# Performance work log

Hardware: AMD Instinct MI355X
Metric: run time of the kernel (lower is better)

## Reference

```python
import jax, jax.numpy as jnp
import numpy as np

NUM_CLIPS = 64
# (kernel, stride) per layer for each scale, per num_scale_layers=[16,8,8]
SCALE_SPECS = [[(1, 1)] + [(2, 1)] * 15,
               [(3, 2)] + [(2, 1)] * 7,
               [(3, 2)] + [(2, 1)] * 7]
KEEP = {0: (7, 15), 1: (3, 7), 2: (3, 5, 7)}


def _build_props():
    # replicates SparsePropMaxPool.__init__ construction of self.props
    tmp = [[1] * 16, [2] + [1] * 7, [2] + [1] * 7]
    acum, stride, props = 0, 1, []
    for scale_idx, strides in enumerate(tmp):
        for i, st in enumerate(strides):
            stride *= st
            if i in KEEP[scale_idx]:
                s = np.arange(0, NUM_CLIPS - acum - i * stride, stride)
                props.append(np.stack([s, s + acum + i * stride], -1))
        acum += stride * (len(strides) + 1)
    props = np.concatenate(props, 0)
    props[:, 1] += 1
    return props.astype(np.int64)  # [153, 2]


def _maxpool1d(x, k, s):
    if k == 1 and s == 1:
        return x
    return jax.lax.reduce_window(x, -jnp.inf, jax.lax.max,
                                 (1, 1, k), (1, 1, s), 'VALID')


def _forward(x, props):
    B, H, N = x.shape  # N == 64
    acum, stride = 0, 1
    s_parts, e_parts, feat_parts = [], [], []
    for scale in SCALE_SPECS:
        for i, (k, st) in enumerate(scale):
            stride *= st
            x = _maxpool1d(x, k, st)
            s = np.arange(0, N - acum - i * stride, stride)
            s_parts.append(s)
            e_parts.append(s + acum + i * stride)
            feat_parts.append(x)  # [B, H, len(s)]
        acum += stride * (len(scale) + 1)
    # all (s,e) diagonals are disjoint across layers -> one fused scatter
    s_all = np.concatenate(s_parts)
    e_all = np.concatenate(e_parts)
    feats = jnp.concatenate(feat_parts, axis=-1)  # [B, H, total]
    ori_map_h = jnp.zeros((B, H, N, N), x.dtype).at[:, :, s_all, e_all].set(feats)
    ori_map_mask = jnp.zeros((B, 1, N, N), x.dtype).at[:, :, s_all, e_all].set(1.0)
    p0, p1 = props[:, 0], props[:, 1] - 1
    props_h = jnp.transpose(ori_map_h[:, :, p0, p1], (0, 2, 1))  # [B, P, H]
    # faithful (no-op) write-back as in the torch source
    ori_map_h = ori_map_h.at[:, :, p0, p1].set(jnp.transpose(props_h, (0, 2, 1)))
    return props_h, ori_map_h, ori_map_mask


def setup_inputs() -> dict:
    key = jax.random.key(0)
    kx, kg = jax.random.split(key)
    x = jax.random.normal(kx, (64, 512, 64), dtype=jnp.float32)
    props = jnp.asarray(_build_props())  # [153, 2]
    props_graph = jax.random.randint(kg, (153, 153), 0, 2, dtype=jnp.int32)
    return {'x': x, 'props': props, 'props_graph': props_graph}


def reference(x, props, props_graph):
    return _forward(x, props)
```

## Files before the change

kernel.cpp:

```cpp
#include <hip/hip_runtime.h>


#define B_ 64
#define H_ 512
#define N_ 64
#define NPROP 153

typedef float f4 __attribute__((ext_vector_type(4)));

__device__ __forceinline__ bool in_set(int s, int d) {
    if (d < 0) return false;
    if (d <= 15) return true;
    if (d <= 31) return (d & 1) && ((s & 1) == 0);
    return (d >= 35) && ((d & 3) == 3) && ((s & 3) == 0);
}

__global__ __launch_bounds__(256) void map_kernel(const float* __restrict__ x,
                                                  float* __restrict__ out_map) {
    const int tid = threadIdx.x;
    const int g   = tid >> 4;
    const int t   = tid & 15;
    const size_t bh = (size_t)blockIdx.x * 16 + g;

    __shared__ __align__(16) float xs[16][72];
    f4 xv = reinterpret_cast<const f4*>(x)[blockIdx.x * 256 + tid];
    *reinterpret_cast<f4*>(&xs[g][4 * t]) = xv;
    __syncthreads();

    f4* mrow = reinterpret_cast<f4*>(out_map + bh * (size_t)(N_ * N_));
    const int e0 = 4 * t;
    float vx = 0.f, vy = 0.f, vz = 0.f, vw = 0.f;
    #pragma unroll
    for (int s = N_ - 1; s >= 0; --s) {
        const float mv = xs[g][s];
        vx = (s == e0 + 0) ? mv : fmaxf(vx, mv);
        vy = (s == e0 + 1) ? mv : fmaxf(vy, mv);
        vz = (s == e0 + 2) ? mv : fmaxf(vz, mv);
        vw = (s == e0 + 3) ? mv : fmaxf(vw, mv);
        f4 w;
        w.x = in_set(s, e0 + 0 - s) ? vx : 0.f;
        w.y = in_set(s, e0 + 1 - s) ? vy : 0.f;
        w.z = in_set(s, e0 + 2 - s) ? vz : 0.f;
        w.w = in_set(s, e0 + 3 - s) ? vw : 0.f;
        __builtin_nontemporal_store(w, &mrow[s * 16 + t]);
    }
}

__global__ __launch_bounds__(64) void props_kernel(const float* __restrict__ x,
                                                   float* __restrict__ out_props,
                                                   float* __restrict__ out_mask) {
    const int lane = threadIdx.x;
    const int b = blockIdx.x >> 3;
    const int c = blockIdx.x & 7;
    const int h = c * 64 + lane;

    const f4* xr = reinterpret_cast<const f4*>(x + ((size_t)b * H_ + h) * N_);
    float r[64];
    #pragma unroll
    for (int k = 0; k < 16; ++k) {
        f4 v = xr[k];
        r[4*k+0] = v.x; r[4*k+1] = v.y; r[4*k+2] = v.z; r[4*k+3] = v.w;
    }
    float a[63];
    #pragma unroll
    for (int i = 0; i < 63; ++i) a[i] = fmaxf(r[i], r[i+1]);
    float bb[61];
    #pragma unroll
    for (int i = 0; i < 61; ++i) bb[i] = fmaxf(a[i], a[i+2]);
    float T3[57];
    #pragma unroll
    for (int i = 0; i < 57; ++i) T3[i] = fmaxf(bb[i], bb[i+4]);

    float* po = out_props + (size_t)b * NPROP * H_ + h;
    int p = 0;
    #pragma unroll
    for (int s = 0; s < 57; ++s)
        __builtin_nontemporal_store(T3[s], &po[(size_t)(p++) * H_]);
    #pragma unroll
    for (int s = 0; s < 49; ++s)
        __builtin_nontemporal_store(fmaxf(T3[s], T3[s + 8]), &po[(size_t)(p++) * H_]);
    #pragma unroll
    for (int s = 0; s <= 40; s += 2)
        __builtin_nontemporal_store(fmaxf(fmaxf(T3[s], T3[s + 8]), T3[s + 16]),
                                    &po[(size_t)(p++) * H_]);
    #pragma unroll
    for (int s = 0; s <= 32; s += 2)
        __builtin_nontemporal_store(
            fmaxf(fmaxf(T3[s], T3[s + 8]), fmaxf(T3[s + 16], T3[s + 24])),
            &po[(size_t)(p++) * H_]);
    #pragma unroll
    for (int s = 0; s <= 16; s += 4) {
        float m = T3[s];
        #pragma unroll
        for (int j = 8; j <= 40; j += 8) m = fmaxf(m, T3[s + j]);
        __builtin_nontemporal_store(m, &po[(size_t)(p++) * H_]);
    }
    #pragma unroll
    for (int s = 0; s <= 8; s += 4) {
        float m = T3[s];
        #pragma unroll
        for (int j = 8; j <= 48; j += 8) m = fmaxf(m, T3[s + j]);
        __builtin_nontemporal_store(m, &po[(size_t)(p++) * H_]);
    }
    {
        float m = T3[0];
        #pragma unroll
        for (int j = 8; j <= 56; j += 8) m = fmaxf(m, T3[j]);
        __builtin_nontemporal_store(m, &po[(size_t)p * H_]);
    }

    if (c == 0) {
        float* mk = out_mask + (size_t)b * (N_ * N_);
        #pragma unroll
        for (int s = 0; s < N_; ++s)
            mk[s * N_ + lane] = in_set(s, lane - s) ? 1.0f : 0.0f;
    }
}

extern "C" void kernel_launch(void* const* d_in, const int* in_sizes, int n_in,
                              void* d_out, int out_size, void* d_ws, size_t ws_size,
                              hipStream_t stream) {
    const float* x = (const float*)d_in[0];
    float* out       = (float*)d_out;
    float* out_props = out;
    float* out_map   = out + (size_t)B_ * NPROP * H_;
    float* out_mask  = out_map + (size_t)B_ * H_ * N_ * N_;

    props_kernel<<<dim3(B_ * (H_ / 64)), dim3(64), 0, stream>>>(x, out_props, out_mask);
    map_kernel<<<dim3(B_ * H_ / 16), dim3(256), 0, stream>>>(x, out_map);
}
```

Before: 106.3 us.

## Fuse props/mask and map kernels into a single launch with block-role split

Merges the props/mask kernel and the map kernel into one launch. The first B blocks compute the mask and the props for a full batch row, two h values per thread, and the remaining blocks write the dense map. This removes a second kernel launch and the serialization between the two kernels, so props work can overlap with the bandwidth-bound map writes. The cost is that the register-heavy props code now shares one kernel with the map path, which can lower occupancy, and the props blocks do twice the serial work per thread.

```diff
diff --git a/kernel.cpp b/kernel.cpp
--- a/kernel.cpp
+++ b/kernel.cpp
@@ -15,15 +15,99 @@
     return (d >= 35) && ((d & 3) == 3) && ((s & 3) == 0);
 }
 
-__global__ __launch_bounds__(256) void map_kernel(const float* __restrict__ x,
-                                                  float* __restrict__ out_map) {
+__global__ __launch_bounds__(256) void fused_kernel(const float* __restrict__ x,
+                                                    float* __restrict__ out_props,
+                                                    float* __restrict__ out_map,
+                                                    float* __restrict__ out_mask) {
     const int tid = threadIdx.x;
-    const int g   = tid >> 4;
-    const int t   = tid & 15;
-    const size_t bh = (size_t)blockIdx.x * 16 + g;
+    const int bid = blockIdx.x;
 
     __shared__ __align__(16) float xs[16][72];
-    f4 xv = reinterpret_cast<const f4*>(x)[blockIdx.x * 256 + tid];
+
+    if (bid < B_) {
+        const int b = bid;
+
+        f4* mk = reinterpret_cast<f4*>(out_mask + (size_t)b * (N_ * N_));
+        #pragma unroll
+        for (int i = 0; i < 4; ++i) {
+            const int idx = tid + 256 * i;
+            const int s = idx >> 4, c = idx & 15;
+            f4 w;
+            w.x = in_set(s, 4 * c + 0 - s) ? 1.f : 0.f;
+            w.y = in_set(s, 4 * c + 1 - s) ? 1.f : 0.f;
+            w.z = in_set(s, 4 * c + 2 - s) ? 1.f : 0.f;
+            w.w = in_set(s, 4 * c + 3 - s) ? 1.f : 0.f;
+            __builtin_nontemporal_store(w, &mk[idx]);
+        }
+
+        #pragma unroll 1
+        for (int half = 0; half < 2; ++half) {
+            const int h = tid + 256 * half;
+            const f4* xr = reinterpret_cast<const f4*>(x + ((size_t)b * H_ + h) * N_);
+            float r[64];
+            #pragma unroll
+            for (int k = 0; k < 16; ++k) {
+                f4 v = xr[k];
+                r[4*k+0] = v.x; r[4*k+1] = v.y; r[4*k+2] = v.z; r[4*k+3] = v.w;
+            }
+            float a[63];
+            #pragma unroll
+            for (int i = 0; i < 63; ++i) a[i] = fmaxf(r[i], r[i+1]);
+            float m4[61];
+            #pragma unroll
+            for (int i = 0; i < 61; ++i) m4[i] = fmaxf(a[i], a[i+2]);
+            float T3[57];
+            #pragma unroll
+            for (int i = 0; i < 57; ++i) T3[i] = fmaxf(m4[i], m4[i+4]);
+
+            float* po = out_props + (size_t)b * NPROP * H_ + h;
+            int p = 0;
+            #pragma unroll
+            for (int s = 0; s < 57; ++s)
+                __builtin_nontemporal_store(T3[s], &po[(size_t)(p++) * H_]);
+            #pragma unroll
+            for (int s = 0; s < 49; ++s)
+                __builtin_nontemporal_store(fmaxf(T3[s], T3[s + 8]),
+                                            &po[(size_t)(p++) * H_]);
+            #pragma unroll
+            for (int s = 0; s <= 40; s += 2)
+                __builtin_nontemporal_store(fmaxf(fmaxf(T3[s], T3[s + 8]), T3[s + 16]),
+                                            &po[(size_t)(p++) * H_]);
+            #pragma unroll
+            for (int s = 0; s <= 32; s += 2)
+                __builtin_nontemporal_store(
+                    fmaxf(fmaxf(T3[s], T3[s + 8]), fmaxf(T3[s + 16], T3[s + 24])),
+                    &po[(size_t)(p++) * H_]);
+            #pragma unroll
+            for (int s = 0; s <= 16; s += 4) {
+                float m = T3[s];
+                #pragma unroll
+                for (int j = 8; j <= 40; j += 8) m = fmaxf(m, T3[s + j]);
+                __builtin_nontemporal_store(m, &po[(size_t)(p++) * H_]);
+            }
+            #pragma unroll
+            for (int s = 0; s <= 8; s += 4) {
+                float m = T3[s];
+                #pragma unroll
+                for (int j = 8; j <= 48; j += 8) m = fmaxf(m, T3[s + j]);
+                __builtin_nontemporal_store(m, &po[(size_t)(p++) * H_]);
+            }
+            {
+                float m = T3[0];
+                #pragma unroll
+                for (int j = 8; j <= 56; j += 8) m = fmaxf(m, T3[j]);
+                __builtin_nontemporal_store(m, &po[(size_t)p * H_]);
+            }
+        }
+        return;
+    }
+
+    const int mb = bid - B_;
+    const int g  = tid >> 4;
+    const int t  = tid & 15;
+    const size_t bh = (size_t)mb * 16 + g;
+
+    f4 xv = reinterpret_cast<const f4*>(x)[mb * 256 + tid];
     *reinterpret_cast<f4*>(&xs[g][4 * t]) = xv;
     __syncthreads();
 
@@ -46,77 +130,6 @@
     }
 }
 
-__global__ __launch_bounds__(64) void props_kernel(const float* __restrict__ x,
-                                                   float* __restrict__ out_props,
-                                                   float* __restrict__ out_mask) {
-    const int lane = threadIdx.x;
-    const int b = blockIdx.x >> 3;
-    const int c = blockIdx.x & 7;
-    const int h = c * 64 + lane;
-
-    const f4* xr = reinterpret_cast<const f4*>(x + ((size_t)b * H_ + h) * N_);
-    float r[64];
-    #pragma unroll
-    for (int k = 0; k < 16; ++k) {
-        f4 v = xr[k];
-        r[4*k+0] = v.x; r[4*k+1] = v.y; r[4*k+2] = v.z; r[4*k+3] = v.w;
-    }
-    float a[63];
-    #pragma unroll
-    for (int i = 0; i < 63; ++i) a[i] = fmaxf(r[i], r[i+1]);
-    float bb[61];
-    #pragma unroll
-    for (int i = 0; i < 61; ++i) bb[i] = fmaxf(a[i], a[i+2]);
-    float T3[57];
-    #pragma unroll
-    for (int i = 0; i < 57; ++i) T3[i] = fmaxf(bb[i], bb[i+4]);
-
-    float* po = out_props + (size_t)b * NPROP * H_ + h;
-    int p = 0;
-    #pragma unroll
-    for (int s = 0; s < 57; ++s)
-        __builtin_nontemporal_store(T3[s], &po[(size_t)(p++) * H_]);
-    #pragma unroll
-    for (int s = 0; s < 49; ++s)
-        __builtin_nontemporal_store(fmaxf(T3[s], T3[s + 8]), &po[(size_t)(p++) * H_]);
-    #pragma unroll
-    for (int s = 0; s <= 40; s += 2)
-        __builtin_nontemporal_store(fmaxf(fmaxf(T3[s], T3[s + 8]), T3[s + 16]),
-                                    &po[(size_t)(p++) * H_]);
-    #pragma unroll
-    for (int s = 0; s <= 32; s += 2)
-        __builtin_nontemporal_store(
-            fmaxf(fmaxf(T3[s], T3[s + 8]), fmaxf(T3[s + 16], T3[s + 24])),
-            &po[(size_t)(p++) * H_]);
-    #pragma unroll
-    for (int s = 0; s <= 16; s += 4) {
-        float m = T3[s];
-        #pragma unroll
-        for (int j = 8; j <= 40; j += 8) m = fmaxf(m, T3[s + j]);
-        __builtin_nontemporal_store(m, &po[(size_t)(p++) * H_]);
-    }
-    #pragma unroll
-    for (int s = 0; s <= 8; s += 4) {
-        float m = T3[s];
-        #pragma unroll
-        for (int j = 8; j <= 48; j += 8) m = fmaxf(m, T3[s + j]);
-        __builtin_nontemporal_store(m, &po[(size_t)(p++) * H_]);
-    }
-    {
-        float m = T3[0];
-        #pragma unroll
-        for (int j = 8; j <= 56; j += 8) m = fmaxf(m, T3[j]);
-        __builtin_nontemporal_store(m, &po[(size_t)p * H_]);
-    }
-
-    if (c == 0) {
-        float* mk = out_mask + (size_t)b * (N_ * N_);
-        #pragma unroll
-        for (int s = 0; s < N_; ++s)
-            mk[s * N_ + lane] = in_set(s, lane - s) ? 1.0f : 0.0f;
-    }
-}
-
 extern "C" void kernel_launch(void* const* d_in, const int* in_sizes, int n_in,
                               void* d_out, int out_size, void* d_ws, size_t ws_size,
                               hipStream_t stream) {
@@ -126,6 +139,6 @@
     float* out_map   = out + (size_t)B_ * NPROP * H_;
     float* out_mask  = out_map + (size_t)B_ * H_ * N_ * N_;
 
-    props_kernel<<<dim3(B_ * (H_ / 64)), dim3(64), 0, stream>>>(x, out_props, out_mask);
-    map_kernel<<<dim3(B_ * H_ / 16), dim3(256), 0, stream>>>(x, out_map);
+    fused_kernel<<<dim3(B_ + B_ * H_ / 16), dim3(256), 0, stream>>>(
+        x, out_props, out_map, out_mask);
 }
```

Result: faster. 101.5 us (-4.5%).
